# Performance work log

Measured on AMD Instinct MI355X. Metric: run time of the kernel, lower is better.

Reference implementation:

```python
import jax, jax.numpy as jnp
import numpy as np

N = 50000      # nodes
E = 800000     # edges
IN = 128       # in_channels
H = 128        # hidden_channels
C = 40         # num_classes
L = 2          # num_layers
BN_EPS = 1e-5


def setup_inputs() -> dict:
    key = jax.random.key(0)
    ks = jax.random.split(key, 16)
    s = 0.02
    return {
        "x": jax.random.normal(ks[0], (N, IN), dtype=jnp.float32),
        "edge_index": jax.random.randint(ks[1], (2, E), 0, N, dtype=jnp.int64),
        "fc0_w": jax.random.normal(ks[2], (H, IN), dtype=jnp.float32) * s,
        "fc0_b": jnp.zeros((H,), dtype=jnp.float32),
        "conv_w": jax.random.normal(ks[3], (L, H, H), dtype=jnp.float32) * s,
        "W_w": jax.random.normal(ks[4], (H, H), dtype=jnp.float32) * s,
        "W_b": jnp.zeros((H,), dtype=jnp.float32),
        "bn_gamma": jnp.ones((L + 1, H), dtype=jnp.float32),
        "bn_beta": jnp.zeros((L + 1, H), dtype=jnp.float32),
        "fc_out_w": jax.random.normal(ks[5], (H, H), dtype=jnp.float32) * s,
        "fc_out_b": jnp.zeros((H,), dtype=jnp.float32),
        "out_w": jax.random.normal(ks[6], (C, H), dtype=jnp.float32) * s,
        "out_b": jnp.zeros((C,), dtype=jnp.float32),
    }


def _bn_eval(x, gamma, beta):
    # eval-mode BatchNorm1d with default running stats (mean=0, var=1)
    return x * (gamma / jnp.sqrt(1.0 + BN_EPS)) + beta


def _gcn_conv(x, w, src, dst, norm, n):
    # x' = D^{-1/2} (A + I) D^{-1/2} (x @ w^T), bias=False
    xw = x @ w.T                        # [N, H]
    msg = xw[src] * norm[:, None]       # [E+N, H] gather + scale
    return jax.ops.segment_sum(msg, dst, num_segments=n)


def reference(x, edge_index, fc0_w, fc0_b, conv_w, W_w, W_b, bn_gamma, bn_beta,
              fc_out_w, fc_out_b, out_w, out_b):
    n = x.shape[0]
    loops = jnp.arange(n, dtype=edge_index.dtype)
    src = jnp.concatenate([edge_index[0], loops])   # add self-loops
    dst = jnp.concatenate([edge_index[1], loops])
    deg = jax.ops.segment_sum(jnp.ones_like(dst, dtype=x.dtype), dst, num_segments=n)
    deg_isqrt = jax.lax.rsqrt(deg)                  # deg >= 1 (self-loops)
    norm = deg_isqrt[src] * deg_isqrt[dst]          # [E+N]

    h = x @ fc0_w.T + fc0_b
    h = _bn_eval(h, bn_gamma[0], bn_beta[0])
    h = jax.nn.relu(h)                              # dropout: eval mode -> identity

    jk = h
    for i in range(L):
        h = _gcn_conv(h, conv_w[i], src, dst, norm, n)
        h = h @ W_w.T + W_b
        h = _bn_eval(h, bn_gamma[i + 1], bn_beta[i + 1])
        h = jax.nn.relu(h)
        jk = jnp.maximum(jk, h)                     # JumpingKnowledge 'max'

    out = jk @ fc_out_w.T + fc_out_b
    return out @ out_w.T + out_b
```

## Files before the change

kernel.cpp:

```cpp
#include <hip/hip_runtime.h>

#define NN 50000
#define NE 800000
#define EN 850000
#define NB 196
#define BINBLK 391
#define CAPE 5120
#define CAPT 5376
#define MMBLK 1563

static constexpr float BN_SC = 0.99999500003749968f;

typedef __bf16 bf16x8 __attribute__((ext_vector_type(8)));
typedef float  f32x4  __attribute__((ext_vector_type(4)));

__device__ __forceinline__ float4 ld4(const float* p){ return *reinterpret_cast<const float4*>(p); }

__device__ __forceinline__ unsigned short f2bf(float f){
  union { float f; unsigned int i; } v; v.f = f;
  unsigned int r = v.i + 0x7fffu + ((v.i >> 16) & 1u);
  return (unsigned short)(r >> 16);
}
__device__ __forceinline__ float lo2f(unsigned int u){
  union { unsigned int i; float f; } v; v.i = u << 16; return v.f;
}
__device__ __forceinline__ float hi2f(unsigned int u){
  union { unsigned int i; float f; } v; v.i = u & 0xffff0000u; return v.f;
}
__device__ __forceinline__ unsigned int pk2(float flo, float fhi){
  return (unsigned int)f2bf(flo) | ((unsigned int)f2bf(fhi) << 16);
}
__device__ __forceinline__ int fragidx(int n, int k){
  int nt = n >> 4, c = n & 15, ks = k >> 5, g = (k >> 3) & 3, j = k & 7;
  return ((nt*4 + ks)*64 + g*16 + c)*8 + j;
}

extern "C" __global__ __launch_bounds__(256)
void k_prep(const float* __restrict__ fc0_w,
            const float* __restrict__ Ww, const float* __restrict__ cw,
            const float* __restrict__ ow, const float* __restrict__ fw,
            const float* __restrict__ fb, const float* __restrict__ ob,
            const int* __restrict__ ei,
            unsigned short* __restrict__ W0f, unsigned short* __restrict__ WC0f,
            unsigned short* __restrict__ WC1f, unsigned short* __restrict__ Wff,
            float* __restrict__ bfv, int* __restrict__ hists, int* __restrict__ gcur){
  int b = blockIdx.x;
  int t = threadIdx.x;
  if (b < 64){
    int idx = b*256 + t;
    int f = idx >> 7, k = idx & 127;
    W0f[fragidx(f, k)] = f2bf(fc0_w[f*128 + k]);
  } else if (b < 192){
    int idx = (b & 63)*256 + t;
    int f = idx >> 7, k = idx & 127;
    const float* c = (b < 128) ? cw : (cw + 16384);
    float acc = 0.f;
    #pragma unroll 4
    for (int j = 0; j < 128; ++j) acc = fmaf(Ww[f*128 + j], c[j*128 + k], acc);
    unsigned short* o = (b < 128) ? WC0f : WC1f;
    o[fragidx(f, k)] = f2bf(acc);
  } else if (b < 216){
    int idx = (b - 192)*256 + t;
    int c = idx >> 7, k = idx & 127;
    float acc = 0.f;
    if (c < 40){
      for (int j = 0; j < 128; ++j) acc = fmaf(ow[c*128 + j], fw[j*128 + k], acc);
    }
    Wff[fragidx(c, k)] = f2bf(acc);
    if (idx < 48){
      float a2 = 0.f;
      if (idx < 40){
        a2 = ob[idx];
        for (int j = 0; j < 128; ++j) a2 = fmaf(ow[idx*128 + j], fb[j], a2);
      }
      bfv[idx] = a2;
    }
  } else {
    __shared__ int h[NB];
    int bb = b - 216;
    if (t < NB) h[t] = 0;
    if (bb == 0 && t < NB) gcur[t] = t*CAPE;
    __syncthreads();
    int e0 = bb*2048;
    for (int i = t; i < 2048; i += 256){
      int e = e0 + i;
      if (e < NE) atomicAdd(&h[ei[NE+e] >> 8], 1);
    }
    __syncthreads();
    if (t < NB) hists[bb*NB + t] = h[t];
  }
}

__device__ __forceinline__ void bin_body(int bb, int t, char* smem,
    const int* __restrict__ ei, const int* __restrict__ hists,
    int* __restrict__ gcur, unsigned int* __restrict__ bbuf){
  int* lbase = (int*)smem;
  int* gbase = lbase + NB;
  int* hcur  = gbase + NB;
  int* totp  = hcur + NB;
  unsigned int* stage = (unsigned int*)(totp + 1);
  unsigned char* bid = (unsigned char*)(stage + 2048);
  int h = (t < NB) ? hists[bb*NB + t] : 0;
  if (t < NB) lbase[t] = h;
  __syncthreads();
  if (t == 0){
    int run = 0;
    for (int b = 0; b < NB; ++b){ int x = lbase[b]; lbase[b] = run; run += x; }
    *totp = run;
  }
  __syncthreads();
  if (t < NB && h > 0) gbase[t] = atomicAdd(&gcur[t], h);
  if (t < NB) hcur[t] = lbase[t];
  __syncthreads();
  int e0 = bb*2048;
  for (int i = t; i < 2048; i += 256){
    int e = e0 + i;
    if (e < NE){
      int s = ei[e], d = ei[NE+e];
      int b = d >> 8;
      int p = atomicAdd(&hcur[b], 1);
      stage[p] = ((unsigned int)d << 16) | (unsigned int)s;
      bid[p] = (unsigned char)b;
    }
  }
  __syncthreads();
  int m = *totp;
  for (int j = t; j < m; j += 256){
    int b = bid[j];
    bbuf[gbase[b] + (j - lbase[b])] = stage[j];
  }
}

template<bool F32>
__device__ __forceinline__ void mm_body(int blk, int t, char* smem,
    const float* __restrict__ Xf, const unsigned short* __restrict__ Xb,
    const unsigned short* __restrict__ Wf, const float* __restrict__ bias,
    const float* __restrict__ gamma, const float* __restrict__ beta,
    unsigned short* __restrict__ Cout){
  unsigned short* eld = (unsigned short*)smem;
  const int lane = t & 63;
  const int wv = t >> 6;
  const int pr = wv >> 1;
  const int nh = wv & 1;
  const int m0 = blk*32 + pr*16;
  const int mrow = min(m0 + (lane & 15), NN-1);
  const int kg = (lane >> 4)*8;
  bf16x8 a[4];
  if constexpr (F32){
    const float* px = Xf + (size_t)mrow*128 + kg;
    #pragma unroll
    for (int ks = 0; ks < 4; ++ks){
      float4 f0 = ld4(px + ks*32);
      float4 f1 = ld4(px + ks*32 + 4);
      bf16x8 aa;
      aa[0]=(__bf16)f0.x; aa[1]=(__bf16)f0.y; aa[2]=(__bf16)f0.z; aa[3]=(__bf16)f0.w;
      aa[4]=(__bf16)f1.x; aa[5]=(__bf16)f1.y; aa[6]=(__bf16)f1.z; aa[7]=(__bf16)f1.w;
      a[ks] = aa;
    }
  } else {
    const unsigned short* px = Xb + (size_t)mrow*128 + kg;
    #pragma unroll
    for (int ks = 0; ks < 4; ++ks)
      a[ks] = *reinterpret_cast<const bf16x8*>(px + ks*32);
  }
  f32x4 acc[4];
  #pragma unroll
  for (int i = 0; i < 4; ++i) acc[i] = (f32x4){0.f,0.f,0.f,0.f};
  #pragma unroll
  for (int ks = 0; ks < 4; ++ks){
    #pragma unroll
    for (int ntl = 0; ntl < 4; ++ntl){
      int nt = nh*4 + ntl;
      bf16x8 bfr = *reinterpret_cast<const bf16x8*>(Wf + ((nt*4 + ks)*64 + lane)*8);
      acc[ntl] = __builtin_amdgcn_mfma_f32_16x16x32_bf16(a[ks], bfr, acc[ntl], 0, 0, 0);
    }
  }
  const int cB = lane & 15;
  const int r0 = (lane >> 4)*4;
  #pragma unroll
  for (int ntl = 0; ntl < 4; ++ntl){
    int cb = (nh*4 + ntl)*16 + cB;
    float bi = bias[cb];
    float g  = gamma[cb]*BN_SC;
    float be = beta[cb];
    #pragma unroll
    for (int r = 0; r < 4; ++r){
      float o = fmaxf(fmaf(acc[ntl][r] + bi, g, be), 0.f);
      eld[(pr*16 + r0 + r)*136 + cb] = f2bf(o);
    }
  }
  __syncthreads();
  {
    int row = t >> 3, seg = t & 7;
    int grow = blk*32 + row;
    if (grow < NN){
      const unsigned short* src = eld + row*136 + seg*16;
      uint4* dst = reinterpret_cast<uint4*>(Cout + (size_t)grow*128 + seg*16);
      dst[0] = *reinterpret_cast<const uint4*>(src);
      dst[1] = *reinterpret_cast<const uint4*>(src + 8);
    }
  }
}

extern "C" __global__ __launch_bounds__(256)
void k_mix(const int* __restrict__ ei, const int* __restrict__ hists,
           int* __restrict__ gcur, unsigned int* __restrict__ bbuf,
           const float* __restrict__ x, const unsigned short* __restrict__ W0f,
           const float* __restrict__ bias, const float* __restrict__ gamma,
           const float* __restrict__ beta, unsigned short* __restrict__ H0){
  __shared__ __align__(16) char smem[12608];
  if (blockIdx.x < BINBLK)
    bin_body(blockIdx.x, threadIdx.x, smem, ei, hists, gcur, bbuf);
  else
    mm_body<true>(blockIdx.x - BINBLK, threadIdx.x, smem, x, nullptr, W0f,
                  bias, gamma, beta, H0);
}

extern "C" __global__ __launch_bounds__(256)
void k_mm2(const unsigned short* __restrict__ Xb, const unsigned short* __restrict__ Wf,
           const float* __restrict__ bias, const float* __restrict__ gamma,
           const float* __restrict__ beta, unsigned short* __restrict__ Cout){
  __shared__ __align__(16) char smem[8704];
  mm_body<false>(blockIdx.x, threadIdx.x, smem, nullptr, Xb, Wf, bias, gamma, beta, Cout);
}

extern "C" __global__ __launch_bounds__(256)
void k_csr(const unsigned int* __restrict__ bbuf, const int* __restrict__ gcur,
           unsigned short* __restrict__ csr, int* __restrict__ offs,
           int* __restrict__ deg, float* __restrict__ dis){
  __shared__ int h[256], loff[256], lcur[256];
  __shared__ unsigned short stage[CAPT];
  int t = threadIdx.x;
  int b = blockIdx.x;
  int nb0 = b << 8;
  int BNv = min(256, NN - nb0);
  int ebeg = b*CAPE;
  int m = gcur[b] - ebeg;
  int base = b*CAPT;
  h[t] = (t < BNv) ? 1 : 0;
  __syncthreads();
  for (int i = t; i < m; i += 256)
    atomicAdd(&h[(bbuf[ebeg + i] >> 16) & 255], 1);
  __syncthreads();
  if (t == 0){
    int run = 0;
    for (int n = 0; n < BNv; ++n){ int x = h[n]; loff[n] = run; run += x; }
  }
  __syncthreads();
  if (t < BNv){
    offs[nb0 + t] = base + loff[t];
    deg[nb0 + t] = h[t];
    dis[nb0 + t] = rsqrtf((float)h[t]);
    lcur[t] = loff[t] + 1;
    stage[loff[t]] = (unsigned short)(nb0 + t);
  }
  __syncthreads();
  for (int i = t; i < m; i += 256){
    unsigned int e = bbuf[ebeg + i];
    int p = atomicAdd(&lcur[(e >> 16) & 255], 1);
    stage[p] = (unsigned short)(e & 0xffffu);
  }
  __syncthreads();
  int M = m + BNv;
  for (int j = t; j < M; j += 256) csr[base + j] = stage[j];
}

extern "C" __global__ __launch_bounds__(256)
void k_gather(const unsigned short* __restrict__ Hf, const unsigned short* __restrict__ csr,
              const float* __restrict__ dis, const int* __restrict__ offs,
              const int* __restrict__ deg, unsigned short* __restrict__ Agg){
  int lane = threadIdx.x & 63;
  int node = blockIdx.x*4 + (threadIdx.x >> 6);
  int grp  = lane >> 4;
  int q8   = (lane & 15)*8;
  int start = offs[node];
  int n = deg[node];
  float dn = rsqrtf((float)n);
  float a0=0,a1=0,a2=0,a3=0,a4=0,a5=0,a6=0,a7=0;
  int nm1 = n - 1;
  for (int i = 0; i < n; i += 32){
    int s[8]; float w[8];
    #pragma unroll
    for (int j = 0; j < 8; ++j){
      int k = i + j*4 + grp;
      int c = min(k, nm1);
      s[j] = csr[start + c];
      w[j] = (k < n) ? dis[s[j]] : 0.f;
    }
    uint4 u[8];
    #pragma unroll
    for (int j = 0; j < 8; ++j)
      u[j] = *reinterpret_cast<const uint4*>(Hf + (size_t)s[j]*128 + q8);
    #pragma unroll
    for (int j = 0; j < 8; ++j){
      a0 = fmaf(lo2f(u[j].x), w[j], a0); a1 = fmaf(hi2f(u[j].x), w[j], a1);
      a2 = fmaf(lo2f(u[j].y), w[j], a2); a3 = fmaf(hi2f(u[j].y), w[j], a3);
      a4 = fmaf(lo2f(u[j].z), w[j], a4); a5 = fmaf(hi2f(u[j].z), w[j], a5);
      a6 = fmaf(lo2f(u[j].w), w[j], a6); a7 = fmaf(hi2f(u[j].w), w[j], a7);
    }
  }
  a0 += __shfl_xor(a0, 16); a1 += __shfl_xor(a1, 16);
  a2 += __shfl_xor(a2, 16); a3 += __shfl_xor(a3, 16);
  a4 += __shfl_xor(a4, 16); a5 += __shfl_xor(a5, 16);
  a6 += __shfl_xor(a6, 16); a7 += __shfl_xor(a7, 16);
  a0 += __shfl_xor(a0, 32); a1 += __shfl_xor(a1, 32);
  a2 += __shfl_xor(a2, 32); a3 += __shfl_xor(a3, 32);
  a4 += __shfl_xor(a4, 32); a5 += __shfl_xor(a5, 32);
  a6 += __shfl_xor(a6, 32); a7 += __shfl_xor(a7, 32);
  if (grp == 0){
    uint4 o;
    o.x = pk2(a0*dn, a1*dn);
    o.y = pk2(a2*dn, a3*dn);
    o.z = pk2(a4*dn, a5*dn);
    o.w = pk2(a6*dn, a7*dn);
    *reinterpret_cast<uint4*>(Agg + node*128 + q8) = o;
  }
}

__global__ __launch_bounds__(256)
void k_mmf(const unsigned short* __restrict__ Xb, const unsigned short* __restrict__ Wf,
           const float* __restrict__ bias, const float* __restrict__ gamma,
           const float* __restrict__ beta,
           const unsigned short* __restrict__ H0, const unsigned short* __restrict__ H1,
           const unsigned short* __restrict__ Wff, const float* __restrict__ bfv,
           float* __restrict__ Out){
  __shared__ __align__(16) unsigned short eldA[4][2176];
  const int t = threadIdx.x;
  const int lane = t & 63;
  const int wv = t >> 6;
  const int m0 = blockIdx.x*64 + wv*16;
  const int mrow = min(m0 + (lane & 15), NN-1);
  const int kg = (lane >> 4)*8;
  bf16x8 a[4];
  {
    const unsigned short* px = Xb + (size_t)mrow*128 + kg;
    #pragma unroll
    for (int ks = 0; ks < 4; ++ks)
      a[ks] = *reinterpret_cast<const bf16x8*>(px + ks*32);
  }
  f32x4 acc[8];
  #pragma unroll
  for (int nt = 0; nt < 8; ++nt) acc[nt] = (f32x4){0.f,0.f,0.f,0.f};
  #pragma unroll
  for (int ks = 0; ks < 4; ++ks){
    #pragma unroll
    for (int nt = 0; nt < 8; ++nt){
      bf16x8 bfr = *reinterpret_cast<const bf16x8*>(Wf + ((nt*4 + ks)*64 + lane)*8);
      acc[nt] = __builtin_amdgcn_mfma_f32_16x16x32_bf16(a[ks], bfr, acc[nt], 0, 0, 0);
    }
  }
  const int cB = lane & 15;
  const int r0 = (lane >> 4)*4;
  unsigned short* eld = eldA[wv];
  #pragma unroll
  for (int nt = 0; nt < 8; ++nt){
    int cb = nt*16 + cB;
    float bi = bias[cb];
    float g  = gamma[cb]*BN_SC;
    float be = beta[cb];
    #pragma unroll
    for (int r = 0; r < 4; ++r){
      float o = fmaxf(fmaf(acc[nt][r] + bi, g, be), 0.f);
      eld[(r0 + r)*136 + cb] = f2bf(o);
    }
  }
  const size_t pb = (size_t)mrow*128 + kg;
  const unsigned short* eldr = eld + (lane & 15)*136 + kg;
  bf16x8 af[4];
  #pragma unroll
  for (int ks = 0; ks < 4; ++ks){
    union U { uint4 v; unsigned short s[8]; } u0, u1, u2, r;
    u0.v = *reinterpret_cast<const uint4*>(H0 + pb + ks*32);
    u1.v = *reinterpret_cast<const uint4*>(H1 + pb + ks*32);
    u2.v = *reinterpret_cast<const uint4*>(eldr + ks*32);
    #pragma unroll
    for (int j = 0; j < 8; ++j){
      unsigned short m = u0.s[j] > u1.s[j] ? u0.s[j] : u1.s[j];
      r.s[j] = m > u2.s[j] ? m : u2.s[j];
    }
    af[ks] = *reinterpret_cast<bf16x8*>(&r);
  }
  f32x4 acc2[3];
  #pragma unroll
  for (int nt = 0; nt < 3; ++nt) acc2[nt] = (f32x4){0.f,0.f,0.f,0.f};
  #pragma unroll
  for (int ks = 0; ks < 4; ++ks){
    #pragma unroll
    for (int nt = 0; nt < 3; ++nt){
      bf16x8 bfr = *reinterpret_cast<const bf16x8*>(Wff + ((nt*4 + ks)*64 + lane)*8);
      acc2[nt] = __builtin_amdgcn_mfma_f32_16x16x32_bf16(af[ks], bfr, acc2[nt], 0, 0, 0);
    }
  }
  #pragma unroll
  for (int nt = 0; nt < 3; ++nt){
    int cb = nt*16 + cB;
    if (cb < 40){
      float bi = bfv[cb];
      #pragma unroll
      for (int r = 0; r < 4; ++r){
        int row = m0 + r0 + r;
        if (row < NN) Out[(size_t)row*40 + cb] = acc2[nt][r] + bi;
      }
    }
  }
}

extern "C" void kernel_launch(void* const* d_in, const int* in_sizes, int n_in,
                              void* d_out, int out_size, void* d_ws, size_t ws_size,
                              hipStream_t stream){
  const float* x     = (const float*)d_in[0];
  const int*   ei    = (const int*)d_in[1];
  const float* fc0_w = (const float*)d_in[2];
  const float* fc0_b = (const float*)d_in[3];
  const float* convw = (const float*)d_in[4];
  const float* Ww    = (const float*)d_in[5];
  const float* Wb    = (const float*)d_in[6];
  const float* bng   = (const float*)d_in[7];
  const float* bnb   = (const float*)d_in[8];
  const float* fow   = (const float*)d_in[9];
  const float* fob   = (const float*)d_in[10];
  const float* outw  = (const float*)d_in[11];
  const float* outb  = (const float*)d_in[12];
  float* out = (float*)d_out;

  char* p = (char*)d_ws;
  auto alloc = [&](size_t n){ char* r = p; p += (n + 255) & ~(size_t)255; return r; };
  int*   hists   = (int*)  alloc((size_t)BINBLK*NB*4);
  int*   gcur    = (int*)  alloc((size_t)NB*4);
  unsigned int*   bbuf  = (unsigned int*)  alloc((size_t)NB*CAPE*4);
  unsigned short* csr16 = (unsigned short*)alloc((size_t)NB*CAPT*2);
  int*   offs    = (int*)  alloc((size_t)NN*4);
  int*   deg     = (int*)  alloc((size_t)NN*4);
  float* dis     = (float*)alloc((size_t)NN*4);
  unsigned short* W0f  = (unsigned short*)alloc(16384*2);
  unsigned short* WC0f = (unsigned short*)alloc(16384*2);
  unsigned short* WC1f = (unsigned short*)alloc(16384*2);
  unsigned short* Wff  = (unsigned short*)alloc(6144*2);
  float* bfv     = (float*)alloc(64*4);
  unsigned short* H0  = (unsigned short*)alloc((size_t)NN*128*2);
  unsigned short* H1  = (unsigned short*)alloc((size_t)NN*128*2);
  unsigned short* AGG = (unsigned short*)alloc((size_t)NN*128*2);

  k_prep<<<216 + BINBLK, 256, 0, stream>>>(fc0_w, Ww, convw, outw, fow, fob, outb, ei,
                                           W0f, WC0f, WC1f, Wff, bfv, hists, gcur);
  k_mix<<<BINBLK + MMBLK, 256, 0, stream>>>(ei, hists, gcur, bbuf,
                                            x, W0f, fc0_b, bng, bnb, H0);
  k_csr<<<NB, 256, 0, stream>>>(bbuf, gcur, csr16, offs, deg, dis);

  k_gather<<<12500, 256, 0, stream>>>(H0, csr16, dis, offs, deg, AGG);
  k_mm2<<<MMBLK, 256, 0, stream>>>(AGG, WC0f, Wb, bng + 128, bnb + 128, H1);
  k_gather<<<12500, 256, 0, stream>>>(H1, csr16, dis, offs, deg, AGG);
  k_mmf<<<782, 256, 0, stream>>>(AGG, WC1f, Wb, bng + 256, bnb + 256,
                                 H0, H1, Wff, bfv, out);
}
```

Measured before the change: 143.6 us.

## Fuse destination histogram into binning pass and add short-degree gather path

Moves the per-block destination-bin histogram out of the prep kernel and into bin_body, so each binning block counts its own edges in shared memory just before scattering. This removes the hists workspace array and its global write and read round-trip, and shrinks the prep launch. The cost is that the edge destinations are read twice inside k_mix, which lengthens the binning blocks. Separately, the gather kernel gains a fast path for nodes with degree at most 16 that issues only 4 row loads per lane group instead of 8, cutting wasted clamped loads for the common low-degree case.

```diff
diff --git a/kernel.cpp b/kernel.cpp
--- a/kernel.cpp
+++ b/kernel.cpp
@@ -40,12 +40,12 @@
             const float* __restrict__ Ww, const float* __restrict__ cw,
             const float* __restrict__ ow, const float* __restrict__ fw,
             const float* __restrict__ fb, const float* __restrict__ ob,
-            const int* __restrict__ ei,
             unsigned short* __restrict__ W0f, unsigned short* __restrict__ WC0f,
             unsigned short* __restrict__ WC1f, unsigned short* __restrict__ Wff,
-            float* __restrict__ bfv, int* __restrict__ hists, int* __restrict__ gcur){
+            float* __restrict__ bfv, int* __restrict__ gcur){
   int b = blockIdx.x;
   int t = threadIdx.x;
+  if (b == 0 && t < NB) gcur[t] = t*CAPE;
   if (b < 64){
     int idx = b*256 + t;
     int f = idx >> 7, k = idx & 127;
@@ -59,7 +59,7 @@
     for (int j = 0; j < 128; ++j) acc = fmaf(Ww[f*128 + j], c[j*128 + k], acc);
     unsigned short* o = (b < 128) ? WC0f : WC1f;
     o[fragidx(f, k)] = f2bf(acc);
-  } else if (b < 216){
+  } else {
     int idx = (b - 192)*256 + t;
     int c = idx >> 7, k = idx & 127;
     float acc = 0.f;
@@ -75,33 +75,26 @@
       }
       bfv[idx] = a2;
     }
-  } else {
-    __shared__ int h[NB];
-    int bb = b - 216;
-    if (t < NB) h[t] = 0;
-    if (bb == 0 && t < NB) gcur[t] = t*CAPE;
-    __syncthreads();
-    int e0 = bb*2048;
-    for (int i = t; i < 2048; i += 256){
-      int e = e0 + i;
-      if (e < NE) atomicAdd(&h[ei[NE+e] >> 8], 1);
-    }
-    __syncthreads();
-    if (t < NB) hists[bb*NB + t] = h[t];
   }
 }
 
 __device__ __forceinline__ void bin_body(int bb, int t, char* smem,
-    const int* __restrict__ ei, const int* __restrict__ hists,
-    int* __restrict__ gcur, unsigned int* __restrict__ bbuf){
+    const int* __restrict__ ei, int* __restrict__ gcur, unsigned int* __restrict__ bbuf){
   int* lbase = (int*)smem;
   int* gbase = lbase + NB;
   int* hcur  = gbase + NB;
   int* totp  = hcur + NB;
   unsigned int* stage = (unsigned int*)(totp + 1);
   unsigned char* bid = (unsigned char*)(stage + 2048);
-  int h = (t < NB) ? hists[bb*NB + t] : 0;
-  if (t < NB) lbase[t] = h;
+  if (t < NB) lbase[t] = 0;
+  __syncthreads();
+  int e0 = bb*2048;
+  for (int i = t; i < 2048; i += 256){
+    int e = e0 + i;
+    if (e < NE) atomicAdd(&lbase[ei[NE+e] >> 8], 1);
+  }
+  __syncthreads();
+  int h = (t < NB) ? lbase[t] : 0;
   __syncthreads();
   if (t == 0){
     int run = 0;
@@ -112,7 +105,6 @@
   if (t < NB && h > 0) gbase[t] = atomicAdd(&gcur[t], h);
   if (t < NB) hcur[t] = lbase[t];
   __syncthreads();
-  int e0 = bb*2048;
   for (int i = t; i < 2048; i += 256){
     int e = e0 + i;
     if (e < NE){
@@ -203,14 +195,14 @@
 }
 
 extern "C" __global__ __launch_bounds__(256)
-void k_mix(const int* __restrict__ ei, const int* __restrict__ hists,
-           int* __restrict__ gcur, unsigned int* __restrict__ bbuf,
+void k_mix(const int* __restrict__ ei, int* __restrict__ gcur,
+           unsigned int* __restrict__ bbuf,
            const float* __restrict__ x, const unsigned short* __restrict__ W0f,
            const float* __restrict__ bias, const float* __restrict__ gamma,
            const float* __restrict__ beta, unsigned short* __restrict__ H0){
   __shared__ __align__(16) char smem[12608];
   if (blockIdx.x < BINBLK)
-    bin_body(blockIdx.x, threadIdx.x, smem, ei, hists, gcur, bbuf);
+    bin_body(blockIdx.x, threadIdx.x, smem, ei, gcur, bbuf);
   else
     mm_body<true>(blockIdx.x - BINBLK, threadIdx.x, smem, x, nullptr, W0f,
                   bias, gamma, beta, H0);
@@ -278,25 +270,47 @@
   float dn = rsqrtf((float)n);
   float a0=0,a1=0,a2=0,a3=0,a4=0,a5=0,a6=0,a7=0;
   int nm1 = n - 1;
-  for (int i = 0; i < n; i += 32){
-    int s[8]; float w[8];
-    #pragma unroll
-    for (int j = 0; j < 8; ++j){
-      int k = i + j*4 + grp;
+  if (n <= 16){
+    int s[4]; float w[4];
+    #pragma unroll
+    for (int j = 0; j < 4; ++j){
+      int k = j*4 + grp;
       int c = min(k, nm1);
       s[j] = csr[start + c];
       w[j] = (k < n) ? dis[s[j]] : 0.f;
     }
-    uint4 u[8];
-    #pragma unroll
-    for (int j = 0; j < 8; ++j)
+    uint4 u[4];
+    #pragma unroll
+    for (int j = 0; j < 4; ++j)
       u[j] = *reinterpret_cast<const uint4*>(Hf + (size_t)s[j]*128 + q8);
     #pragma unroll
-    for (int j = 0; j < 8; ++j){
+    for (int j = 0; j < 4; ++j){
       a0 = fmaf(lo2f(u[j].x), w[j], a0); a1 = fmaf(hi2f(u[j].x), w[j], a1);
       a2 = fmaf(lo2f(u[j].y), w[j], a2); a3 = fmaf(hi2f(u[j].y), w[j], a3);
       a4 = fmaf(lo2f(u[j].z), w[j], a4); a5 = fmaf(hi2f(u[j].z), w[j], a5);
       a6 = fmaf(lo2f(u[j].w), w[j], a6); a7 = fmaf(hi2f(u[j].w), w[j], a7);
+    }
+  } else {
+    for (int i = 0; i < n; i += 32){
+      int s[8]; float w[8];
+      #pragma unroll
+      for (int j = 0; j < 8; ++j){
+        int k = i + j*4 + grp;
+        int c = min(k, nm1);
+        s[j] = csr[start + c];
+        w[j] = (k < n) ? dis[s[j]] : 0.f;
+      }
+      uint4 u[8];
+      #pragma unroll
+      for (int j = 0; j < 8; ++j)
+        u[j] = *reinterpret_cast<const uint4*>(Hf + (size_t)s[j]*128 + q8);
+      #pragma unroll
+      for (int j = 0; j < 8; ++j){
+        a0 = fmaf(lo2f(u[j].x), w[j], a0); a1 = fmaf(hi2f(u[j].x), w[j], a1);
+        a2 = fmaf(lo2f(u[j].y), w[j], a2); a3 = fmaf(hi2f(u[j].y), w[j], a3);
+        a4 = fmaf(lo2f(u[j].z), w[j], a4); a5 = fmaf(hi2f(u[j].z), w[j], a5);
+        a6 = fmaf(lo2f(u[j].w), w[j], a6); a7 = fmaf(hi2f(u[j].w), w[j], a7);
+      }
     }
   }
   a0 += __shfl_xor(a0, 16); a1 += __shfl_xor(a1, 16);
@@ -425,7 +439,6 @@
 
   char* p = (char*)d_ws;
   auto alloc = [&](size_t n){ char* r = p; p += (n + 255) & ~(size_t)255; return r; };
-  int*   hists   = (int*)  alloc((size_t)BINBLK*NB*4);
   int*   gcur    = (int*)  alloc((size_t)NB*4);
   unsigned int*   bbuf  = (unsigned int*)  alloc((size_t)NB*CAPE*4);
   unsigned short* csr16 = (unsigned short*)alloc((size_t)NB*CAPT*2);
@@ -441,9 +454,9 @@
   unsigned short* H1  = (unsigned short*)alloc((size_t)NN*128*2);
   unsigned short* AGG = (unsigned short*)alloc((size_t)NN*128*2);
 
-  k_prep<<<216 + BINBLK, 256, 0, stream>>>(fc0_w, Ww, convw, outw, fow, fob, outb, ei,
-                                           W0f, WC0f, WC1f, Wff, bfv, hists, gcur);
-  k_mix<<<BINBLK + MMBLK, 256, 0, stream>>>(ei, hists, gcur, bbuf,
+  k_prep<<<216, 256, 0, stream>>>(fc0_w, Ww, convw, outw, fow, fob, outb,
+                                  W0f, WC0f, WC1f, Wff, bfv, gcur);
+  k_mix<<<BINBLK + MMBLK, 256, 0, stream>>>(ei, gcur, bbuf,
                                             x, W0f, fc0_b, bng, bnb, H0);
   k_csr<<<NB, 256, 0, stream>>>(bbuf, gcur, csr16, offs, deg, dis);
 
```

Result: faster. 137.3 us (-4.4%).
